# Optimization experiments

Hardware: AMD Instinct MI355X
Metric: run time of the kernel (lower is better)

## Reference

```python
import math
import jax, jax.numpy as jnp
import numpy as np

B = 8192           # batch_size
N = 256            # num_features (n_tokens)
D = 64             # embedding_dim (even)
H = D // 2         # half dim for sin/cos coefficients


def setup_inputs() -> dict:
    key = jax.random.key(0)
    k1, k2, k3 = jax.random.split(key, 3)
    inputs = jax.random.normal(k1, (B, N), dtype=jnp.float32)
    # coef initialized with stddev=sigma (sigma=1.0)
    coef = jax.random.normal(k2, (1, N, H), dtype=jnp.float32)
    weight = jax.random.normal(k3, (1, N, D, D), dtype=jnp.float32)
    bias = jnp.zeros((1, N, D), dtype=jnp.float32)
    return {"inputs": inputs, "coef": coef, "weight": weight, "bias": bias}


def reference(inputs, coef, weight, bias):
    # v: [B, N, H]
    v = (2.0 * math.pi) * coef * inputs[..., None]
    emb = jnp.concatenate([jnp.sin(v), jnp.cos(v)], axis=-1)  # [B, N, D]
    # per-token linear: one DxD matmul per token (NLinear), done as batched einsum
    emb = jnp.einsum('bni,nio->bno', emb, weight[0]) + bias    # [B, N, D]
    emb = jax.nn.relu(emb)
    return emb.reshape(-1, N * D)                              # [B, N*D]
```

## Files before the change

### kernel.cpp

```cpp
#include <hip/hip_runtime.h>


typedef short bf16x8 __attribute__((ext_vector_type(8)));
typedef float f32x4 __attribute__((ext_vector_type(4)));

#define BM   128
#define LDW  72

__device__ __forceinline__ short f2bf(float f) {
    unsigned u = __float_as_uint(f);
    unsigned r = (u + 0x7FFFu + ((u >> 16) & 1u)) >> 16;
    return (short)r;
}

__global__ __launch_bounds__(256) void pe_mfma_kernel(
    const float* __restrict__ x,
    const float* __restrict__ coef,
    const float* __restrict__ wgt,
    const float* __restrict__ bias,
    float* __restrict__ out)
{
    const int N = 256;

    const int bid = blockIdx.x;
    const int n   = bid & (N - 1);
    const int b0  = (bid >> 8) * BM;

    __shared__ short wt[64 * LDW];

    const int t = threadIdx.x;

    const float* Wn = wgt + n * 4096;
    #pragma unroll
    for (int it = 0; it < 16; ++it) {
        int idx = it * 256 + t;
        int i = idx >> 6, o = idx & 63;
        wt[o * LDW + i] = f2bf(Wn[idx]);
    }
    __syncthreads();

    const int w  = t >> 6;
    const int l  = t & 63;
    const int lr = l & 15;
    const int lg = l >> 4;

    const float* cp = coef + n * 32 + lg * 8;
    float c[8];
    #pragma unroll
    for (int j = 0; j < 8; ++j) c[j] = cp[j];

    const int row0 = b0 + w * 32 + lr;
    const float x0 = x[row0 * N + n];
    const float x1 = x[(row0 + 16) * N + n];

    bf16x8 a_s[2], a_c[2];
    #pragma unroll
    for (int m = 0; m < 2; ++m) {
        float xv = m ? x1 : x0;
        #pragma unroll
        for (int j = 0; j < 8; ++j) {
            float tt = c[j] * xv;
            tt = __builtin_amdgcn_fractf(tt);
            a_s[m][j] = f2bf(__builtin_amdgcn_sinf(tt));
            a_c[m][j] = f2bf(__builtin_amdgcn_cosf(tt));
        }
    }

    bf16x8 bfr[4][2];
    #pragma unroll
    for (int nf = 0; nf < 4; ++nf) {
        int col = nf * 16 + lr;
        #pragma unroll
        for (int ki = 0; ki < 2; ++ki) {
            int k = ki * 32 + lg * 8;
            bfr[nf][ki] = *(const bf16x8*)(&wt[col * LDW + k]);
        }
    }

    f32x4 acc[2][4];
    #pragma unroll
    for (int m = 0; m < 2; ++m)
        #pragma unroll
        for (int nf = 0; nf < 4; ++nf) {
            f32x4 z = {0.f, 0.f, 0.f, 0.f};
            z = __builtin_amdgcn_mfma_f32_16x16x32_bf16(a_s[m], bfr[nf][0], z, 0, 0, 0);
            z = __builtin_amdgcn_mfma_f32_16x16x32_bf16(a_c[m], bfr[nf][1], z, 0, 0, 0);
            acc[m][nf] = z;
        }

    const float* bn = bias + n * 64;
    float bv[4];
    #pragma unroll
    for (int nf = 0; nf < 4; ++nf) bv[nf] = bn[nf * 16 + lr];

    #pragma unroll
    for (int m = 0; m < 2; ++m)
        #pragma unroll
        for (int nf = 0; nf < 4; ++nf) {
            int col = nf * 16 + lr;
            #pragma unroll
            for (int r = 0; r < 4; ++r) {
                int row = b0 + w * 32 + m * 16 + lg * 4 + r;
                float v = acc[m][nf][r] + bv[nf];
                out[(size_t)row * 16384 + n * 64 + col] = fmaxf(v, 0.0f);
            }
        }
}

extern "C" void kernel_launch(void* const* d_in, const int* in_sizes, int n_in,
                              void* d_out, int out_size, void* d_ws, size_t ws_size,
                              hipStream_t stream) {
    const float* x    = (const float*)d_in[0];
    const float* coef = (const float*)d_in[1];
    const float* wgt  = (const float*)d_in[2];
    const float* bias = (const float*)d_in[3];
    float* out = (float*)d_out;

    dim3 grid(256 * (8192 / BM));
    dim3 block(256);
    hipLaunchKernelGGL(pe_mfma_kernel, grid, block, 0, stream,
                       x, coef, wgt, bias, out);
}
```

Before: 108.8 us.

## Pre-pack bf16 weights once in a prologue kernel and vectorize output stores

A separate kernel converts each token's weight matrix to bf16 once, in the exact MFMA fragment order, and writes it to workspace. The main kernel then loads its B fragments straight from global memory with no LDS staging and no barrier. Previously each of the 64 batch blocks per token redid that conversion. The MFMA operands are also swapped so each lane holds four consecutive output columns, which allows 16-byte vector stores and vector bias loads. The cost is an extra launch and a workspace write, with a fallback path kept for when the workspace is too small.

```diff
diff --git a/kernel.cpp b/kernel.cpp
--- a/kernel.cpp
+++ b/kernel.cpp
@@ -4,8 +4,7 @@
 typedef short bf16x8 __attribute__((ext_vector_type(8)));
 typedef float f32x4 __attribute__((ext_vector_type(4)));
 
-#define BM   128
-#define LDW  72
+#define BM 128
 
 __device__ __forceinline__ short f2bf(float f) {
     unsigned u = __float_as_uint(f);
@@ -13,36 +12,66 @@
     return (short)r;
 }
 
-__global__ __launch_bounds__(256) void pe_mfma_kernel(
+__global__ __launch_bounds__(256) void pe_wconv(
+    const float* __restrict__ wgt, short* __restrict__ wt)
+{
+    __shared__ float lw[64 * 65];
+    const int n = blockIdx.x;
+    const int t = threadIdx.x;
+
+    const float4* Wn4 = (const float4*)(wgt + n * 4096);
+    #pragma unroll
+    for (int it = 0; it < 4; ++it) {
+        int idx4 = it * 256 + t;
+        float4 v = Wn4[idx4];
+        int flat = idx4 * 4;
+        int k = flat >> 6, o = flat & 63;
+        lw[k * 65 + o + 0] = v.x;
+        lw[k * 65 + o + 1] = v.y;
+        lw[k * 65 + o + 2] = v.z;
+        lw[k * 65 + o + 3] = v.w;
+    }
+    __syncthreads();
+
+    short* outp = wt + n * 4096;
+    #pragma unroll
+    for (int half = 0; half < 2; ++half) {
+        int c  = half * 256 + t;
+        int lr = c & 15, lg = (c >> 4) & 3, ki = (c >> 6) & 1, nf = c >> 7;
+        int o  = nf * 16 + lr;
+        int kb = ki * 32 + lg * 8;
+        bf16x8 pk;
+        #pragma unroll
+        for (int j = 0; j < 8; ++j) pk[j] = f2bf(lw[(kb + j) * 65 + o]);
+        *(bf16x8*)(outp + c * 8) = pk;
+    }
+}
+
+__global__ __launch_bounds__(256) void pe_main_ws(
     const float* __restrict__ x,
     const float* __restrict__ coef,
-    const float* __restrict__ wgt,
+    const short* __restrict__ wt,
     const float* __restrict__ bias,
     float* __restrict__ out)
 {
     const int N = 256;
-
     const int bid = blockIdx.x;
     const int n   = bid & (N - 1);
     const int b0  = (bid >> 8) * BM;
 
-    __shared__ short wt[64 * LDW];
-
-    const int t = threadIdx.x;
-
-    const float* Wn = wgt + n * 4096;
-    #pragma unroll
-    for (int it = 0; it < 16; ++it) {
-        int idx = it * 256 + t;
-        int i = idx >> 6, o = idx & 63;
-        wt[o * LDW + i] = f2bf(Wn[idx]);
-    }
-    __syncthreads();
-
+    const int t  = threadIdx.x;
     const int w  = t >> 6;
     const int l  = t & 63;
     const int lr = l & 15;
     const int lg = l >> 4;
+
+    const short* wtn = wt + n * 4096;
+    bf16x8 bfr[4][2];
+    #pragma unroll
+    for (int nf = 0; nf < 4; ++nf)
+        #pragma unroll
+        for (int ki = 0; ki < 2; ++ki)
+            bfr[nf][ki] = *(const bf16x8*)(wtn + ((nf * 2 + ki) * 64 + l) * 8);
 
     const float* cp = coef + n * 32 + lg * 8;
     float c[8];
@@ -66,15 +95,92 @@
         }
     }
 
+    f32x4 acc[2][4];
+    #pragma unroll
+    for (int m = 0; m < 2; ++m)
+        #pragma unroll
+        for (int nf = 0; nf < 4; ++nf) {
+            f32x4 z = {0.f, 0.f, 0.f, 0.f};
+            z = __builtin_amdgcn_mfma_f32_16x16x32_bf16(bfr[nf][0], a_s[m], z, 0, 0, 0);
+            z = __builtin_amdgcn_mfma_f32_16x16x32_bf16(bfr[nf][1], a_c[m], z, 0, 0, 0);
+            acc[m][nf] = z;
+        }
+
+    const float* bn = bias + n * 64;
+    f32x4 bv[4];
+    #pragma unroll
+    for (int nf = 0; nf < 4; ++nf)
+        bv[nf] = *(const f32x4*)(bn + nf * 16 + lg * 4);
+
+    #pragma unroll
+    for (int m = 0; m < 2; ++m) {
+        int row = b0 + w * 32 + m * 16 + lr;
+        float* op = out + (size_t)row * 16384 + n * 64 + lg * 4;
+        #pragma unroll
+        for (int nf = 0; nf < 4; ++nf) {
+            f32x4 v = acc[m][nf] + bv[nf];
+            f32x4 r;
+            #pragma unroll
+            for (int q = 0; q < 4; ++q) r[q] = fmaxf(v[q], 0.0f);
+            *(f32x4*)(op + nf * 16) = r;
+        }
+    }
+}
+
+#define LDW 72
+__global__ __launch_bounds__(256) void pe_mfma_fallback(
+    const float* __restrict__ x, const float* __restrict__ coef,
+    const float* __restrict__ wgt, const float* __restrict__ bias,
+    float* __restrict__ out)
+{
+    const int N = 256;
+    const int bid = blockIdx.x;
+    const int n   = bid & (N - 1);
+    const int b0  = (bid >> 8) * BM;
+
+    __shared__ short wtl[64 * LDW];
+    const int t = threadIdx.x;
+
+    const float* Wn = wgt + n * 4096;
+    #pragma unroll
+    for (int it = 0; it < 16; ++it) {
+        int idx = it * 256 + t;
+        int i = idx >> 6, o = idx & 63;
+        wtl[o * LDW + i] = f2bf(Wn[idx]);
+    }
+    __syncthreads();
+
+    const int w = t >> 6, l = t & 63, lr = l & 15, lg = l >> 4;
+
+    const float* cp = coef + n * 32 + lg * 8;
+    float c[8];
+    #pragma unroll
+    for (int j = 0; j < 8; ++j) c[j] = cp[j];
+
+    const int row0 = b0 + w * 32 + lr;
+    const float x0 = x[row0 * N + n];
+    const float x1 = x[(row0 + 16) * N + n];
+
+    bf16x8 a_s[2], a_c[2];
+    #pragma unroll
+    for (int m = 0; m < 2; ++m) {
+        float xv = m ? x1 : x0;
+        #pragma unroll
+        for (int j = 0; j < 8; ++j) {
+            float tt = c[j] * xv;
+            tt = __builtin_amdgcn_fractf(tt);
+            a_s[m][j] = f2bf(__builtin_amdgcn_sinf(tt));
+            a_c[m][j] = f2bf(__builtin_amdgcn_cosf(tt));
+        }
+    }
+
     bf16x8 bfr[4][2];
     #pragma unroll
     for (int nf = 0; nf < 4; ++nf) {
         int col = nf * 16 + lr;
         #pragma unroll
-        for (int ki = 0; ki < 2; ++ki) {
-            int k = ki * 32 + lg * 8;
-            bfr[nf][ki] = *(const bf16x8*)(&wt[col * LDW + k]);
-        }
+        for (int ki = 0; ki < 2; ++ki)
+            bfr[nf][ki] = *(const bf16x8*)(&wtl[col * LDW + ki * 32 + lg * 8]);
     }
 
     f32x4 acc[2][4];
@@ -83,28 +189,30 @@
         #pragma unroll
         for (int nf = 0; nf < 4; ++nf) {
             f32x4 z = {0.f, 0.f, 0.f, 0.f};
-            z = __builtin_amdgcn_mfma_f32_16x16x32_bf16(a_s[m], bfr[nf][0], z, 0, 0, 0);
-            z = __builtin_amdgcn_mfma_f32_16x16x32_bf16(a_c[m], bfr[nf][1], z, 0, 0, 0);
+            z = __builtin_amdgcn_mfma_f32_16x16x32_bf16(bfr[nf][0], a_s[m], z, 0, 0, 0);
+            z = __builtin_amdgcn_mfma_f32_16x16x32_bf16(bfr[nf][1], a_c[m], z, 0, 0, 0);
             acc[m][nf] = z;
         }
 
     const float* bn = bias + n * 64;
-    float bv[4];
-    #pragma unroll
-    for (int nf = 0; nf < 4; ++nf) bv[nf] = bn[nf * 16 + lr];
-
-    #pragma unroll
-    for (int m = 0; m < 2; ++m)
-        #pragma unroll
-        for (int nf = 0; nf < 4; ++nf) {
-            int col = nf * 16 + lr;
+    f32x4 bv[4];
+    #pragma unroll
+    for (int nf = 0; nf < 4; ++nf)
+        bv[nf] = *(const f32x4*)(bn + nf * 16 + lg * 4);
+
+    #pragma unroll
+    for (int m = 0; m < 2; ++m) {
+        int row = b0 + w * 32 + m * 16 + lr;
+        float* op = out + (size_t)row * 16384 + n * 64 + lg * 4;
+        #pragma unroll
+        for (int nf = 0; nf < 4; ++nf) {
+            f32x4 v = acc[m][nf] + bv[nf];
+            f32x4 r;
             #pragma unroll
-            for (int r = 0; r < 4; ++r) {
-                int row = b0 + w * 32 + m * 16 + lg * 4 + r;
-                float v = acc[m][nf][r] + bv[nf];
-                out[(size_t)row * 16384 + n * 64 + col] = fmaxf(v, 0.0f);
-            }
-        }
+            for (int q = 0; q < 4; ++q) r[q] = fmaxf(v[q], 0.0f);
+            *(f32x4*)(op + nf * 16) = r;
+        }
+    }
 }
 
 extern "C" void kernel_launch(void* const* d_in, const int* in_sizes, int n_in,
@@ -116,8 +224,14 @@
     const float* bias = (const float*)d_in[3];
     float* out = (float*)d_out;
 
-    dim3 grid(256 * (8192 / BM));
-    dim3 block(256);
-    hipLaunchKernelGGL(pe_mfma_kernel, grid, block, 0, stream,
-                       x, coef, wgt, bias, out);
-}
+    const size_t wt_bytes = 256 * 4096 * sizeof(short);
+    if (ws_size >= wt_bytes) {
+        short* wt = (short*)d_ws;
+        hipLaunchKernelGGL(pe_wconv, dim3(256), dim3(256), 0, stream, wgt, wt);
+        hipLaunchKernelGGL(pe_main_ws, dim3(256 * (8192 / BM)), dim3(256), 0, stream,
+                           x, coef, (const short*)wt, bias, out);
+    } else {
+        hipLaunchKernelGGL(pe_mfma_fallback, dim3(256 * (8192 / BM)), dim3(256), 0, stream,
+                           x, coef, wgt, bias, out);
+    }
+}
```

Result: slower. 164.4 us (+51.1%).

## Loop each block over four batch tiles and vectorize output stores

Applied to the files above, without the earlier changes.

Each block now processes four 128-row batch tiles for the same token, so the per-token weight conversion into LDS and the fragment loads are amortized over four tiles. The grid shrinks fourfold to match. The MFMA operand order is swapped, which transposes the accumulator layout so each lane holds four consecutive output columns and can write them as a single 16-byte vector store instead of scalar strided stores. Fewer blocks may reduce latency hiding, since each block now runs a serial loop.

```diff
diff --git a/kernel.cpp b/kernel.cpp
--- a/kernel.cpp
+++ b/kernel.cpp
@@ -4,8 +4,9 @@
 typedef short bf16x8 __attribute__((ext_vector_type(8)));
 typedef float f32x4 __attribute__((ext_vector_type(4)));
 
-#define BM   128
-#define LDW  72
+#define BM    128
+#define TILES 4
+#define LDW   72
 
 __device__ __forceinline__ short f2bf(float f) {
     unsigned u = __float_as_uint(f);
@@ -13,7 +14,7 @@
     return (short)r;
 }
 
-__global__ __launch_bounds__(256) void pe_mfma_kernel(
+__global__ __launch_bounds__(256) void pe_kernel(
     const float* __restrict__ x,
     const float* __restrict__ coef,
     const float* __restrict__ wgt,
@@ -21,13 +22,11 @@
     float* __restrict__ out)
 {
     const int N = 256;
+    const int bid = blockIdx.x;
+    const int n      = bid & (N - 1);
+    const int b_base = (bid >> 8) * (BM * TILES);
 
-    const int bid = blockIdx.x;
-    const int n   = bid & (N - 1);
-    const int b0  = (bid >> 8) * BM;
-
-    __shared__ short wt[64 * LDW];
-
+    __shared__ short wtl[64 * LDW];
     const int t = threadIdx.x;
 
     const float* Wn = wgt + n * 4096;
@@ -35,7 +34,7 @@
     for (int it = 0; it < 16; ++it) {
         int idx = it * 256 + t;
         int i = idx >> 6, o = idx & 63;
-        wt[o * LDW + i] = f2bf(Wn[idx]);
+        wtl[o * LDW + i] = f2bf(Wn[idx]);
     }
     __syncthreads();
 
@@ -44,67 +43,68 @@
     const int lr = l & 15;
     const int lg = l >> 4;
 
+    bf16x8 bfr[4][2];
+    #pragma unroll
+    for (int nf = 0; nf < 4; ++nf)
+        #pragma unroll
+        for (int ki = 0; ki < 2; ++ki)
+            bfr[nf][ki] = *(const bf16x8*)(&wtl[(nf * 16 + lr) * LDW + ki * 32 + lg * 8]);
+
     const float* cp = coef + n * 32 + lg * 8;
     float c[8];
     #pragma unroll
     for (int j = 0; j < 8; ++j) c[j] = cp[j];
 
-    const int row0 = b0 + w * 32 + lr;
-    const float x0 = x[row0 * N + n];
-    const float x1 = x[(row0 + 16) * N + n];
+    const float* bn = bias + n * 64;
+    f32x4 bv[4];
+    #pragma unroll
+    for (int nf = 0; nf < 4; ++nf)
+        bv[nf] = *(const f32x4*)(bn + nf * 16 + lg * 4);
 
-    bf16x8 a_s[2], a_c[2];
-    #pragma unroll
-    for (int m = 0; m < 2; ++m) {
-        float xv = m ? x1 : x0;
+    for (int tt = 0; tt < TILES; ++tt) {
+        const int b0   = b_base + tt * BM;
+        const int row0 = b0 + w * 32 + lr;
+        const float x0 = x[row0 * N + n];
+        const float x1 = x[(row0 + 16) * N + n];
+
+        bf16x8 a_s[2], a_c[2];
         #pragma unroll
-        for (int j = 0; j < 8; ++j) {
-            float tt = c[j] * xv;
-            tt = __builtin_amdgcn_fractf(tt);
-            a_s[m][j] = f2bf(__builtin_amdgcn_sinf(tt));
-            a_c[m][j] = f2bf(__builtin_amdgcn_cosf(tt));
+        for (int m = 0; m < 2; ++m) {
+            float xv = m ? x1 : x0;
+            #pragma unroll
+            for (int j = 0; j < 8; ++j) {
+                float v = c[j] * xv;
+                v = __builtin_amdgcn_fractf(v);
+                a_s[m][j] = f2bf(__builtin_amdgcn_sinf(v));
+                a_c[m][j] = f2bf(__builtin_amdgcn_cosf(v));
+            }
+        }
+
+        f32x4 acc[2][4];
+        #pragma unroll
+        for (int m = 0; m < 2; ++m)
+            #pragma unroll
+            for (int nf = 0; nf < 4; ++nf) {
+                f32x4 z = {0.f, 0.f, 0.f, 0.f};
+                z = __builtin_amdgcn_mfma_f32_16x16x32_bf16(bfr[nf][0], a_s[m], z, 0, 0, 0);
+                z = __builtin_amdgcn_mfma_f32_16x16x32_bf16(bfr[nf][1], a_c[m], z, 0, 0, 0);
+                acc[m][nf] = z;
+            }
+
+        #pragma unroll
+        for (int m = 0; m < 2; ++m) {
+            int row = b0 + w * 32 + m * 16 + lr;
+            float* op = out + (size_t)row * 16384 + n * 64 + lg * 4;
+            #pragma unroll
+            for (int nf = 0; nf < 4; ++nf) {
+                f32x4 v = acc[m][nf] + bv[nf];
+                f32x4 r;
+                #pragma unroll
+                for (int q = 0; q < 4; ++q) r[q] = fmaxf(v[q], 0.0f);
+                *(f32x4*)(op + nf * 16) = r;
+            }
         }
     }
-
-    bf16x8 bfr[4][2];
-    #pragma unroll
-    for (int nf = 0; nf < 4; ++nf) {
-        int col = nf * 16 + lr;
-        #pragma unroll
-        for (int ki = 0; ki < 2; ++ki) {
-            int k = ki * 32 + lg * 8;
-            bfr[nf][ki] = *(const bf16x8*)(&wt[col * LDW + k]);
-        }
-    }
-
-    f32x4 acc[2][4];
-    #pragma unroll
-    for (int m = 0; m < 2; ++m)
-        #pragma unroll
-        for (int nf = 0; nf < 4; ++nf) {
-            f32x4 z = {0.f, 0.f, 0.f, 0.f};
-            z = __builtin_amdgcn_mfma_f32_16x16x32_bf16(a_s[m], bfr[nf][0], z, 0, 0, 0);
-            z = __builtin_amdgcn_mfma_f32_16x16x32_bf16(a_c[m], bfr[nf][1], z, 0, 0, 0);
-            acc[m][nf] = z;
-        }
-
-    const float* bn = bias + n * 64;
-    float bv[4];
-    #pragma unroll
-    for (int nf = 0; nf < 4; ++nf) bv[nf] = bn[nf * 16 + lr];
-
-    #pragma unroll
-    for (int m = 0; m < 2; ++m)
-        #pragma unroll
-        for (int nf = 0; nf < 4; ++nf) {
-            int col = nf * 16 + lr;
-            #pragma unroll
-            for (int r = 0; r < 4; ++r) {
-                int row = b0 + w * 32 + m * 16 + lg * 4 + r;
-                float v = acc[m][nf][r] + bv[nf];
-                out[(size_t)row * 16384 + n * 64 + col] = fmaxf(v, 0.0f);
-            }
-        }
 }
 
 extern "C" void kernel_launch(void* const* d_in, const int* in_sizes, int n_in,
@@ -116,8 +116,8 @@
     const float* bias = (const float*)d_in[3];
     float* out = (float*)d_out;
 
-    dim3 grid(256 * (8192 / BM));
+    dim3 grid(256 * (8192 / (BM * TILES)));
     dim3 block(256);
-    hipLaunchKernelGGL(pe_mfma_kernel, grid, block, 0, stream,
+    hipLaunchKernelGGL(pe_kernel, grid, block, 0, stream,
                        x, coef, wgt, bias, out);
 }
```

New measurement: 108.4 us. Within noise of the previous version (-0.4%).
